# Kernel optimization log

Hardware: AMD Instinct MI355X
Metric: run time of the kernel (lower is better)

The kernel has to match this reference:

```python
import jax, jax.numpy as jnp
import numpy as np
import math

B, N, F, H, T = 2, 1024, 8, 64, 16
E_R, E_C, EA = 8192, 32768, 4
NF = N * F


def _pos_enc(t_steps, h):
    pe = np.zeros((t_steps, h), dtype=np.float32)
    pos = np.arange(t_steps, dtype=np.float32)[:, None]
    div = np.exp(np.arange(0, h, 2, dtype=np.float32) * -(math.log(10000.0) / h))
    pe[:, 0::2] = np.sin(pos * div)
    pe[:, 1::2] = np.cos(pos * div)
    return jnp.asarray(pe)


def _ln(x, g, b, eps=1e-5):
    m = x.mean(-1, keepdims=True)
    v = jnp.var(x, axis=-1, keepdims=True)
    return (x - m) / jnp.sqrt(v + eps) * g + b


def _lrelu(x):
    return jnp.where(x >= 0, x, 0.01 * x)


def setup_inputs() -> dict:
    key = jax.random.key(0)
    ks = jax.random.split(key, 40)
    s = 0.05
    inp = {
        'x_global': jax.random.normal(ks[0], (B, N, H, T), jnp.float32),
        'per_feature_x': jax.random.normal(ks[1], (B, N, F, H, T), jnp.float32),
        'river_edge_attr': jax.random.uniform(ks[2], (E_R, EA), jnp.float32),
        'causal_edge_weight': jax.random.uniform(ks[3], (E_C,), jnp.float32),
        'W_tc': jax.random.normal(ks[4], (H, H, 3), jnp.float32) * s,
        'b_tc': jnp.zeros((H,), jnp.float32),
        'r_lin_W': jax.random.normal(ks[5], (H, H), jnp.float32) * s,
        'r_lin_b': jnp.zeros((H,), jnp.float32),
        'r_upd_W': jax.random.normal(ks[6], (2 * H, H), jnp.float32) * s,
        'r_upd_b': jnp.zeros((H,), jnp.float32),
        'r_edge_W': jax.random.normal(ks[7], (EA, 1), jnp.float32) * s,
        'r_edge_b': jnp.zeros((1,), jnp.float32),
        'r_gate': jnp.ones((1,), jnp.float32) * 0.3,
        'c_lin_W': jax.random.normal(ks[8], (H, H), jnp.float32) * s,
        'c_lin_b': jnp.zeros((H,), jnp.float32),
        'c_upd_W': jax.random.normal(ks[9], (2 * H, H), jnp.float32) * s,
        'c_upd_b': jnp.zeros((H,), jnp.float32),
        'c_gate': jnp.ones((1,), jnp.float32) * 0.3,
        'sf_W': jax.random.normal(ks[10], (2 * H, H), jnp.float32) * s,
        'sf_b': jnp.zeros((H,), jnp.float32),
        'femb': jax.random.normal(ks[11], (F, H), jnp.float32) * 0.02,
        'pfn_g': jnp.ones((H,), jnp.float32),
        'pfn_b': jnp.zeros((H,), jnp.float32),
        'f1_W': jax.random.normal(ks[12], (2 * H, H), jnp.float32) * s,
        'f1_b': jnp.zeros((H,), jnp.float32),
        'fln_g': jnp.ones((H,), jnp.float32),
        'fln_b': jnp.zeros((H,), jnp.float32),
        'f2_W': jax.random.normal(ks[13], (H, H), jnp.float32) * s,
        'f2_b': jnp.zeros((H,), jnp.float32),
        'river_edge_index': jax.random.randint(ks[14], (2, E_R), 0, N, jnp.int64),
        'causal_edge_index': jax.random.randint(ks[15], (2, E_C), 0, NF, jnp.int64),
    }
    return inp


def reference(x_global, per_feature_x, river_edge_attr, causal_edge_weight,
              W_tc, b_tc, r_lin_W, r_lin_b, r_upd_W, r_upd_b, r_edge_W, r_edge_b, r_gate,
              c_lin_W, c_lin_b, c_upd_W, c_upd_b, c_gate, sf_W, sf_b, femb,
              pfn_g, pfn_b, f1_W, f1_b, fln_g, fln_b, f2_W, f2_b,
              river_edge_index, causal_edge_index):
    b_, n_, h_, t_ = x_global.shape
    f_ = per_feature_x.shape[2]
    nf = n_ * f_

    # ---- river graph conv (vectorized over B,T) ----
    x_bt = jnp.transpose(x_global, (0, 3, 1, 2))  # [B,T,N,H]
    ew = (river_edge_attr @ r_edge_W + r_edge_b)[:, 0]  # edge_encoder -> [E_r]
    mw_r = jnp.clip(jax.nn.sigmoid(r_gate) * ew, 0.0, 1.0)
    src_r, tgt_r = river_edge_index[0], river_edge_index[1]
    lx = x_bt @ r_lin_W + r_lin_b
    msg_r = lx[:, :, src_r, :] * mw_r[None, None, :, None]  # [B,T,E_r,H]
    agg_r = jnp.zeros_like(x_bt).at[:, :, tgt_r, :].add(msg_r)
    river_upd = _lrelu(jnp.concatenate([agg_r, x_bt], -1) @ r_upd_W + r_upd_b)

    # ---- causal graph conv on (basin, feature) nodes ----
    pf_bt = jnp.transpose(per_feature_x, (0, 4, 1, 2, 3))  # [B,T,N,F,H]
    nodes = (pf_bt + femb[None, None, None]).reshape(b_, t_, nf, h_)
    mw_c = jnp.clip(jax.nn.sigmoid(c_gate) * causal_edge_weight, 0.0, 1.0)
    src_c, tgt_c = causal_edge_index[0], causal_edge_index[1]
    clx = nodes @ c_lin_W + c_lin_b
    msg_c = clx[:, :, src_c, :] * mw_c[None, None, :, None]  # [B,T,E_c,H]
    agg_c = jnp.zeros_like(nodes).at[:, :, tgt_c, :].add(msg_c)
    cupd = _lrelu(jnp.concatenate([agg_c, nodes], -1) @ c_upd_W + c_upd_b)
    cupd = cupd.reshape(b_, t_, n_, f_, h_)

    # per-feature layernorm over H, then to [B,N,F,H,T]
    pf_out = _ln(cupd, pfn_g, pfn_b)
    pf_out = jnp.transpose(pf_out, (0, 2, 3, 4, 1))

    causal_pooled = cupd.mean(axis=3)  # [B,T,N,H]
    x_spatial = jax.nn.silu(jnp.concatenate([river_upd, causal_pooled], -1) @ sf_W + sf_b)

    # ---- temporal conv with sin/cos positional encoding ----
    pe = _pos_enc(t_, h_)
    xt = jnp.transpose(x_global, (0, 1, 3, 2)) + pe[None, None]  # [B,N,T,H]
    x_nch = jnp.transpose(xt.reshape(b_ * n_, t_, h_), (0, 2, 1))  # [BN,H,T]
    y = jax.lax.conv_general_dilated(x_nch, W_tc, (1,), [(1, 1)],
                                     dimension_numbers=('NCH', 'OIH', 'NCH'))
    y = y + b_tc[None, :, None]
    x_temporal = jnp.transpose(y, (0, 2, 1)).reshape(b_, n_, t_, h_)

    # ---- fusion ----
    x_sp_bnth = jnp.transpose(x_spatial, (0, 2, 1, 3))  # [B,N,T,H]
    fz = jnp.concatenate([x_temporal, x_sp_bnth], -1) @ f1_W + f1_b
    fz = jax.nn.silu(_ln(fz, fln_g, fln_b))
    fz = fz @ f2_W + f2_b
    x_out = jnp.transpose(fz, (0, 1, 3, 2))  # [B,N,H,T]
    return (x_out, pf_out)
```

## Files before the change

### kernel.cpp

```cpp
#include <hip/hip_runtime.h>
#include <cstddef>

#define BB 2
#define NN 1024
#define FF 8
#define HH 64
#define TT 16
#define ER 8192
#define EC 32768
#define EA 4
#define NFD 8192
#define BTT 32
#define LDA 68

__device__ __forceinline__ void tile_gemm(const float* At, const float* Wt,
                                          float4 acc[4], int r0, int c0) {
#pragma unroll 8
  for (int k = 0; k < 64; ++k) {
    float4 a = *(const float4*)(At + k * LDA + r0);
    float4 b = *(const float4*)(Wt + k * LDA + c0);
    acc[0].x = fmaf(a.x, b.x, acc[0].x); acc[0].y = fmaf(a.x, b.y, acc[0].y);
    acc[0].z = fmaf(a.x, b.z, acc[0].z); acc[0].w = fmaf(a.x, b.w, acc[0].w);
    acc[1].x = fmaf(a.y, b.x, acc[1].x); acc[1].y = fmaf(a.y, b.y, acc[1].y);
    acc[1].z = fmaf(a.y, b.z, acc[1].z); acc[1].w = fmaf(a.y, b.w, acc[1].w);
    acc[2].x = fmaf(a.z, b.x, acc[2].x); acc[2].y = fmaf(a.z, b.y, acc[2].y);
    acc[2].z = fmaf(a.z, b.z, acc[2].z); acc[2].w = fmaf(a.z, b.w, acc[2].w);
    acc[3].x = fmaf(a.w, b.x, acc[3].x); acc[3].y = fmaf(a.w, b.y, acc[3].y);
    acc[3].z = fmaf(a.w, b.z, acc[3].z); acc[3].w = fmaf(a.w, b.w, acc[3].w);
  }
}

__device__ __forceinline__ void stage_W(float* Wt, const float* __restrict__ W, int tid) {
#pragma unroll
  for (int q = 0; q < 4; ++q) {
    int i = tid + q * 256;
    int k = i >> 4, c4 = (i & 15) << 2;
    *(float4*)(Wt + k * LDA + c4) = *(const float4*)(W + k * 64 + c4);
  }
}

__device__ __forceinline__ void stage_AT(float* At, const float* __restrict__ src, int tid) {
  int row = tid >> 2, kc = (tid & 3) << 4;
  if (src) {
#pragma unroll
    for (int q = 0; q < 4; ++q) {
      float4 v = *(const float4*)(src + kc + q * 4);
      int k = kc + q * 4;
      At[(k + 0) * LDA + row] = v.x;
      At[(k + 1) * LDA + row] = v.y;
      At[(k + 2) * LDA + row] = v.z;
      At[(k + 3) * LDA + row] = v.w;
    }
  } else {
#pragma unroll
    for (int q = 0; q < 16; ++q) At[(kc + q) * LDA + row] = 0.f;
  }
}

#define FMA4(P, V) \
  P.x = fmaf(w, V.x, P.x); P.y = fmaf(w, V.y, P.y); \
  P.z = fmaf(w, V.z, P.z); P.w = fmaf(w, V.w, P.w);

__device__ __forceinline__ void stage_gather(float* At, float* s_sh,
                                             const float* __restrict__ slice, int rowbase,
                                             const float* __restrict__ mw,
                                             const int* __restrict__ srcarr,
                                             const int* __restrict__ off,
                                             const int* __restrict__ sorted, int tid) {
  int row = tid >> 2, kc = (tid & 3) << 4;
  float4 p0 = make_float4(0.f, 0.f, 0.f, 0.f), p1 = p0, p2 = p0, p3 = p0;
  float s = 0.f;
  int node = rowbase + row;
  int e0 = off[node], e1 = off[node + 1];
  for (int j = e0; j < e1; ++j) {
    int e = sorted[j];
    float w = mw[e];
    const float4* sp = (const float4*)(slice + (size_t)srcarr[e] * 64 + kc);
    float4 v0 = sp[0], v1 = sp[1], v2 = sp[2], v3 = sp[3];
    FMA4(p0, v0); FMA4(p1, v1); FMA4(p2, v2); FMA4(p3, v3);
    s += w;
  }
  At[(kc + 0) * LDA + row] = p0.x;  At[(kc + 1) * LDA + row] = p0.y;
  At[(kc + 2) * LDA + row] = p0.z;  At[(kc + 3) * LDA + row] = p0.w;
  At[(kc + 4) * LDA + row] = p1.x;  At[(kc + 5) * LDA + row] = p1.y;
  At[(kc + 6) * LDA + row] = p1.z;  At[(kc + 7) * LDA + row] = p1.w;
  At[(kc + 8) * LDA + row] = p2.x;  At[(kc + 9) * LDA + row] = p2.y;
  At[(kc + 10) * LDA + row] = p2.z; At[(kc + 11) * LDA + row] = p2.w;
  At[(kc + 12) * LDA + row] = p3.x; At[(kc + 13) * LDA + row] = p3.y;
  At[(kc + 14) * LDA + row] = p3.z; At[(kc + 15) * LDA + row] = p3.w;
  if ((tid & 3) == 0) s_sh[row] = s;
}

__global__ __launch_bounds__(256, 4) void k_gnn(const float* __restrict__ base,
    const int* __restrict__ off, const int* __restrict__ sorted,
    const int* __restrict__ srcarr, const float* __restrict__ mw,
    const float* __restrict__ Wf, const float* __restrict__ Wbot,
    const float* __restrict__ vv, const float* __restrict__ bb,
    float* __restrict__ out, int ngShift, int rowsSlice) {
  __shared__ float At[64 * LDA];
  __shared__ float Wt[64 * LDA];
  __shared__ float s_sh[64];
  int tid = threadIdx.x;
  int bt = blockIdx.x >> ngShift;
  int ng = blockIdx.x & ((1 << ngShift) - 1);
  const float* slice = base + (size_t)bt * rowsSlice * 64;
  int rowbase = ng * 64;
  float4 z4 = make_float4(0.f, 0.f, 0.f, 0.f);
  float4 acc[4] = {z4, z4, z4, z4};
  int r0 = (tid >> 4) << 2, c0 = (tid & 15) << 2;

  stage_W(Wt, Wf, tid);
  stage_gather(At, s_sh, slice, rowbase, mw, srcarr, off, sorted, tid);
  __syncthreads();
  tile_gemm(At, Wt, acc, r0, c0);
  __syncthreads();

  stage_W(Wt, Wbot, tid);
  stage_AT(At, slice + (size_t)(rowbase + (tid >> 2)) * 64, tid);
  __syncthreads();
  tile_gemm(At, Wt, acc, r0, c0);

  float4 v4 = *(const float4*)(vv + c0);
  float4 b4 = *(const float4*)(bb + c0);
#pragma unroll
  for (int i = 0; i < 4; ++i) {
    int row = r0 + i;
    float sv = s_sh[row];
    float4 z;
    z.x = acc[i].x + sv * v4.x + b4.x;
    z.y = acc[i].y + sv * v4.y + b4.y;
    z.z = acc[i].z + sv * v4.z + b4.z;
    z.w = acc[i].w + sv * v4.w + b4.w;
    z.x = z.x >= 0.f ? z.x : 0.01f * z.x;
    z.y = z.y >= 0.f ? z.y : 0.01f * z.y;
    z.z = z.z >= 0.f ? z.z : 0.01f * z.z;
    z.w = z.w >= 0.f ? z.w : 0.01f * z.w;
    *(float4*)(out + ((size_t)bt * rowsSlice + rowbase + row) * 64 + c0) = z;
  }
}

__global__ __launch_bounds__(256, 4) void k_sf2(const float* __restrict__ river_upd,
    const float* __restrict__ pooled, const float* __restrict__ sf_W,
    const float* __restrict__ sf_b, float* __restrict__ x_spatial) {
  __shared__ float At[64 * LDA];
  __shared__ float Wt[64 * LDA];
  int tid = threadIdx.x;
  int rowbase = blockIdx.x * 64;
  float4 z4 = make_float4(0.f, 0.f, 0.f, 0.f);
  float4 acc[4] = {z4, z4, z4, z4};
  int r0 = (tid >> 4) << 2, c0 = (tid & 15) << 2;

  stage_W(Wt, sf_W, tid);
  stage_AT(At, river_upd + (size_t)(rowbase + (tid >> 2)) * 64, tid);
  __syncthreads();
  tile_gemm(At, Wt, acc, r0, c0);
  __syncthreads();

  stage_W(Wt, sf_W + 4096, tid);
  stage_AT(At, pooled + (size_t)(rowbase + (tid >> 2)) * 64, tid);
  __syncthreads();
  tile_gemm(At, Wt, acc, r0, c0);

  float4 b4 = *(const float4*)(sf_b + c0);
#pragma unroll
  for (int i = 0; i < 4; ++i) {
    float4 z;
    z.x = acc[i].x + b4.x; z.y = acc[i].y + b4.y;
    z.z = acc[i].z + b4.z; z.w = acc[i].w + b4.w;
    z.x = z.x / (1.f + expf(-z.x)); z.y = z.y / (1.f + expf(-z.y));
    z.z = z.z / (1.f + expf(-z.z)); z.w = z.w / (1.f + expf(-z.w));
    *(float4*)(x_spatial + (size_t)(rowbase + r0 + i) * 64 + c0) = z;
  }
}

__global__ __launch_bounds__(256, 4) void k_fuse2(const float* __restrict__ xt,
    const float* __restrict__ xsp, const float* __restrict__ Wg,
    const float* __restrict__ cvec, const float* __restrict__ f1W,
    const float* __restrict__ flng, const float* __restrict__ flnb,
    const float* __restrict__ f2W, const float* __restrict__ f2b,
    float* __restrict__ x_out) {
  __shared__ float At[64 * LDA];
  __shared__ float Wt[64 * LDA];
  int tid = threadIdx.x;
  int bn0 = blockIdx.x * 4;
  int srow = tid >> 2;
  int bnl = srow >> 4, t = srow & 15;
  int bn = bn0 + bnl;
  float4 z4 = make_float4(0.f, 0.f, 0.f, 0.f);
  float4 acc[4] = {z4, z4, z4, z4};
  int r0 = (tid >> 4) << 2, c0 = (tid & 15) << 2;

#pragma unroll
  for (int kt = 0; kt < 3; ++kt) {
    int t2 = t + kt - 1;
    const float* src = (t2 >= 0 && t2 < TT) ? xt + ((size_t)bn * TT + t2) * 64 : nullptr;
    stage_W(Wt, Wg + kt * 4096, tid);
    stage_AT(At, src, tid);
    __syncthreads();
    tile_gemm(At, Wt, acc, r0, c0);
    __syncthreads();
  }
  {
    int b = bn >> 10, n = bn & 1023;
    const float* src = xsp + ((size_t)(b * TT + t) * NN + n) * 64;
    stage_W(Wt, f1W + 4096, tid);
    stage_AT(At, src, tid);
    __syncthreads();
    tile_gemm(At, Wt, acc, r0, c0);
    __syncthreads();
  }

  float4 cv = *(const float4*)(cvec + c0);
  float4 g4 = *(const float4*)(flng + c0);
  float4 lb4 = *(const float4*)(flnb + c0);
  float4 zz[4];
#pragma unroll
  for (int i = 0; i < 4; ++i) {
    zz[i].x = acc[i].x + cv.x; zz[i].y = acc[i].y + cv.y;
    zz[i].z = acc[i].z + cv.z; zz[i].w = acc[i].w + cv.w;
    float ps = zz[i].x + zz[i].y + zz[i].z + zz[i].w;
    float pq = zz[i].x * zz[i].x + zz[i].y * zz[i].y + zz[i].z * zz[i].z + zz[i].w * zz[i].w;
    ps += __shfl_xor(ps, 1); pq += __shfl_xor(pq, 1);
    ps += __shfl_xor(ps, 2); pq += __shfl_xor(pq, 2);
    ps += __shfl_xor(ps, 4); pq += __shfl_xor(pq, 4);
    ps += __shfl_xor(ps, 8); pq += __shfl_xor(pq, 8);
    float m = ps * (1.f / 64.f);
    float var = pq * (1.f / 64.f) - m * m;
    float inv = rsqrtf(var + 1e-5f);
    float4 w;
    w.x = (zz[i].x - m) * inv * g4.x + lb4.x;
    w.y = (zz[i].y - m) * inv * g4.y + lb4.y;
    w.z = (zz[i].z - m) * inv * g4.z + lb4.z;
    w.w = (zz[i].w - m) * inv * g4.w + lb4.w;
    zz[i].x = w.x / (1.f + expf(-w.x));
    zz[i].y = w.y / (1.f + expf(-w.y));
    zz[i].z = w.z / (1.f + expf(-w.z));
    zz[i].w = w.w / (1.f + expf(-w.w));
  }
#pragma unroll
  for (int i = 0; i < 4; ++i) {
    At[(c0 + 0) * LDA + r0 + i] = zz[i].x;
    At[(c0 + 1) * LDA + r0 + i] = zz[i].y;
    At[(c0 + 2) * LDA + r0 + i] = zz[i].z;
    At[(c0 + 3) * LDA + r0 + i] = zz[i].w;
  }
  stage_W(Wt, f2W, tid);
  __syncthreads();
  float4 acc2[4] = {z4, z4, z4, z4};
  tile_gemm(At, Wt, acc2, r0, c0);
  __syncthreads();
  float4 f2b4 = *(const float4*)(f2b + c0);
#pragma unroll
  for (int i = 0; i < 4; ++i) {
    float4 o;
    o.x = acc2[i].x + f2b4.x; o.y = acc2[i].y + f2b4.y;
    o.z = acc2[i].z + f2b4.z; o.w = acc2[i].w + f2b4.w;
    *(float4*)(Wt + (r0 + i) * LDA + c0) = o;
  }
  __syncthreads();
#pragma unroll
  for (int q = 0; q < 4; ++q) {
    int idx = tid + q * 256;
    int fo = idx * 4;
    int bnl2 = fo >> 10, rem = fo & 1023;
    int c = rem >> 4, tt = rem & 15;
    float4 o;
    o.x = Wt[(bnl2 * 16 + tt + 0) * LDA + c];
    o.y = Wt[(bnl2 * 16 + tt + 1) * LDA + c];
    o.z = Wt[(bnl2 * 16 + tt + 2) * LDA + c];
    o.w = Wt[(bnl2 * 16 + tt + 3) * LDA + c];
    *(float4*)(x_out + (size_t)(bn0 + bnl2) * 1024 + rem) = o;
  }
}

__global__ void k_prep_edges(const float* __restrict__ attr, const float* __restrict__ cw,
                             const float* __restrict__ reW, const float* __restrict__ reB,
                             const float* __restrict__ rgate, const float* __restrict__ cgate,
                             float* __restrict__ mw_r, float* __restrict__ mw_c,
                             int* __restrict__ rcnt, int* __restrict__ ccnt) {
  int i = blockIdx.x * 256 + threadIdx.x;
  if (i < EC) {
    float g = 1.f / (1.f + expf(-cgate[0]));
    mw_c[i] = fminf(fmaxf(g * cw[i], 0.f), 1.f);
  }
  if (i < ER) {
    float ew = reB[0];
#pragma unroll
    for (int a = 0; a < EA; ++a) ew += attr[i * EA + a] * reW[a];
    float g = 1.f / (1.f + expf(-rgate[0]));
    mw_r[i] = fminf(fmaxf(g * ew, 0.f), 1.f);
  }
  if (i < NN) rcnt[i] = 0;
  if (i < NFD) ccnt[i] = 0;
}

__global__ void k_prep_w(const float* __restrict__ r_lin_W, const float* __restrict__ r_upd_W,
                         const float* __restrict__ r_lin_b,
                         const float* __restrict__ c_lin_W, const float* __restrict__ c_upd_W,
                         const float* __restrict__ c_lin_b,
                         const float* __restrict__ W_tc, const float* __restrict__ b_tc,
                         const float* __restrict__ f1_W, const float* __restrict__ f1_b,
                         float* __restrict__ Wfr, float* __restrict__ v_r,
                         float* __restrict__ Wfc, float* __restrict__ v_c,
                         float* __restrict__ Wg, float* __restrict__ cvec) {
  int tid = threadIdx.x;
  if (blockIdx.x == 0) {
    for (int idx = tid; idx < 4096; idx += 256) {
      int k = idx >> 6, j = idx & 63;
      float s = 0.f;
      for (int m = 0; m < 64; ++m) s += r_lin_W[k * 64 + m] * r_upd_W[m * 64 + j];
      Wfr[idx] = s;
    }
    if (tid < 64) {
      float s = 0.f;
      for (int m = 0; m < 64; ++m) s += r_lin_b[m] * r_upd_W[m * 64 + tid];
      v_r[tid] = s;
    }
  } else if (blockIdx.x == 1) {
    for (int idx = tid; idx < 4096; idx += 256) {
      int k = idx >> 6, j = idx & 63;
      float s = 0.f;
      for (int m = 0; m < 64; ++m) s += c_lin_W[k * 64 + m] * c_upd_W[m * 64 + j];
      Wfc[idx] = s;
    }
    if (tid < 64) {
      float s = 0.f;
      for (int m = 0; m < 64; ++m) s += c_lin_b[m] * c_upd_W[m * 64 + tid];
      v_c[tid] = s;
    }
  } else {
    for (int idx = tid; idx < 12288; idx += 256) {
      int r = idx >> 6, c = idx & 63;
      int kk = r >> 6, i = r & 63;
      float s = 0.f;
      for (int o = 0; o < 64; ++o) s += W_tc[o * 192 + i * 3 + kk] * f1_W[o * 64 + c];
      Wg[idx] = s;
    }
    if (tid < 64) {
      float s = f1_b[tid];
      for (int o = 0; o < 64; ++o) s += b_tc[o] * f1_W[o * 64 + tid];
      cvec[tid] = s;
    }
  }
}

__global__ void k_count(const int* __restrict__ ridx, const int* __restrict__ cidx,
                        int* __restrict__ rcnt, int* __restrict__ ccnt) {
  int e = blockIdx.x * 256 + threadIdx.x;
  if (e < ER) atomicAdd(&rcnt[ridx[ER + e]], 1);
  if (e < EC) atomicAdd(&ccnt[cidx[EC + e]], 1);
}

template <int ITEMS>
__device__ __forceinline__ void scan_impl(const int* __restrict__ cnt, int n,
                                          int* __restrict__ off, int* __restrict__ cur,
                                          int* sh) {
  int tid = threadIdx.x;
  int local[ITEMS];
  int s = 0;
  int base = tid * ITEMS;
#pragma unroll
  for (int j = 0; j < ITEMS; ++j) { local[j] = cnt[base + j]; s += local[j]; }
  sh[tid] = s;
  __syncthreads();
  for (int d = 1; d < 1024; d <<= 1) {
    int v = (tid >= d) ? sh[tid - d] : 0;
    __syncthreads();
    sh[tid] += v;
    __syncthreads();
  }
  int excl = tid ? sh[tid - 1] : 0;
#pragma unroll
  for (int j = 0; j < ITEMS; ++j) { off[base + j] = excl; cur[base + j] = excl; excl += local[j]; }
  if (tid == 1023) off[n] = excl;
}

__global__ __launch_bounds__(1024) void k_scan(const int* __restrict__ rcnt, int* __restrict__ roff,
                                               int* __restrict__ rcur,
                                               const int* __restrict__ ccnt, int* __restrict__ coff,
                                               int* __restrict__ ccur) {
  __shared__ int sh[1024];
  if (blockIdx.x == 0) scan_impl<1>(rcnt, NN, roff, rcur, sh);
  else                 scan_impl<8>(ccnt, NFD, coff, ccur, sh);
}

__global__ void k_fill(const int* __restrict__ ridx, const int* __restrict__ cidx,
                       int* __restrict__ rcur, int* __restrict__ ccur,
                       int* __restrict__ rsorted, int* __restrict__ csorted) {
  int e = blockIdx.x * 256 + threadIdx.x;
  if (e < ER) { int t = ridx[ER + e]; int p = atomicAdd(&rcur[t], 1); rsorted[p] = e; }
  if (e < EC) { int t = cidx[EC + e]; int p = atomicAdd(&ccur[t], 1); csorted[p] = e; }
}

__global__ void k_xpose(const float* __restrict__ xg, float* __restrict__ x_bt,
                        float* __restrict__ xt) {
  __shared__ float lds[64][17];
  int bn = blockIdx.x;
  int b = bn >> 10, n = bn & 1023;
  int tid = threadIdx.x;
  const float* src = xg + (size_t)bn * (HH * TT);
  for (int i = tid; i < 1024; i += 256) lds[i >> 4][i & 15] = src[i];
  __syncthreads();
  for (int i = tid; i < 1024; i += 256) {
    int t = i >> 6, h = i & 63;
    float v = lds[h][t];
    float div = expf(-(float)(h & ~1) * (9.210340371976184f / 64.f));
    float arg = (float)t * div;
    float pe = (h & 1) ? cosf(arg) : sinf(arg);
    xt[(size_t)bn * 1024 + i] = v + pe;
    x_bt[(((size_t)b * TT + t) * NN + n) * HH + h] = v;
  }
}

__global__ void k_nodes(const float* __restrict__ pfx, const float* __restrict__ femb,
                        float* __restrict__ nodes) {
  __shared__ float lds[64][17];
  int bnf = blockIdx.x;
  int f = bnf & 7;
  int n = (bnf >> 3) & 1023;
  int b = bnf >> 13;
  int tid = threadIdx.x;
  const float* src = pfx + (size_t)bnf * (HH * TT);
  for (int i = tid; i < 1024; i += 256) lds[i >> 4][i & 15] = src[i];
  __syncthreads();
  for (int i = tid; i < 1024; i += 256) {
    int t = i >> 6, h = i & 63;
    nodes[(((size_t)b * TT + t) * NFD + n * FF + f) * HH + h] = lds[h][t] + femb[f * HH + h];
  }
}

__global__ void k_pool(const float* __restrict__ cupd, float* __restrict__ pooled) {
  int idx = blockIdx.x * 256 + threadIdx.x;
  int h = idx & 63;
  int n = (idx >> 6) & 1023;
  int bt = idx >> 16;
  const float* base = cupd + ((size_t)bt * NFD + n * FF) * HH + h;
  float s = 0.f;
#pragma unroll
  for (int f = 0; f < FF; ++f) s += base[f * HH];
  pooled[idx] = s * 0.125f;
}

__global__ void k_pfout(const float* __restrict__ cupd, const float* __restrict__ g,
                        const float* __restrict__ be, float* __restrict__ pf_out) {
  __shared__ float lds[16][65];
  __shared__ float mi[16], rs[16];
  int bnf = blockIdx.x;
  int f = bnf & 7;
  int n = (bnf >> 3) & 1023;
  int b = bnf >> 13;
  int tid = threadIdx.x;
  for (int i = tid; i < 1024; i += 256) {
    int t = i >> 6, h = i & 63;
    lds[t][h] = cupd[(((size_t)b * TT + t) * NFD + n * FF + f) * HH + h];
  }
  __syncthreads();
  int t = tid >> 4, l = tid & 15;
  float sm = 0.f;
#pragma unroll
  for (int q = 0; q < 4; ++q) sm += lds[t][l + 16 * q];
  sm += __shfl_xor(sm, 1); sm += __shfl_xor(sm, 2); sm += __shfl_xor(sm, 4); sm += __shfl_xor(sm, 8);
  float m = sm * (1.f / 64.f);
  float sv = 0.f;
#pragma unroll
  for (int q = 0; q < 4; ++q) { float d = lds[t][l + 16 * q] - m; sv += d * d; }
  sv += __shfl_xor(sv, 1); sv += __shfl_xor(sv, 2); sv += __shfl_xor(sv, 4); sv += __shfl_xor(sv, 8);
  float inv = 1.f / sqrtf(sv * (1.f / 64.f) + 1e-5f);
  if (l == 0) { mi[t] = m; rs[t] = inv; }
  __syncthreads();
  float* out = pf_out + (size_t)bnf * (HH * TT);
  for (int i = tid; i < 1024; i += 256) {
    int h = i >> 4, tt = i & 15;
    out[i] = (lds[tt][h] - mi[tt]) * rs[tt] * g[h] + be[h];
  }
}

extern "C" void kernel_launch(void* const* d_in, const int* in_sizes, int n_in,
                              void* d_out, int out_size, void* d_ws, size_t ws_size,
                              hipStream_t stream) {
  (void)in_sizes; (void)n_in; (void)out_size; (void)ws_size;
  const float* x_global     = (const float*)d_in[0];
  const float* per_feature  = (const float*)d_in[1];
  const float* r_edge_attr  = (const float*)d_in[2];
  const float* c_edge_w     = (const float*)d_in[3];
  const float* W_tc         = (const float*)d_in[4];
  const float* b_tc         = (const float*)d_in[5];
  const float* r_lin_W      = (const float*)d_in[6];
  const float* r_lin_b      = (const float*)d_in[7];
  const float* r_upd_W      = (const float*)d_in[8];
  const float* r_upd_b      = (const float*)d_in[9];
  const float* r_edge_W     = (const float*)d_in[10];
  const float* r_edge_b     = (const float*)d_in[11];
  const float* r_gate       = (const float*)d_in[12];
  const float* c_lin_W      = (const float*)d_in[13];
  const float* c_lin_b      = (const float*)d_in[14];
  const float* c_upd_W      = (const float*)d_in[15];
  const float* c_upd_b      = (const float*)d_in[16];
  const float* c_gate       = (const float*)d_in[17];
  const float* sf_W         = (const float*)d_in[18];
  const float* sf_b         = (const float*)d_in[19];
  const float* femb         = (const float*)d_in[20];
  const float* pfn_g        = (const float*)d_in[21];
  const float* pfn_b        = (const float*)d_in[22];
  const float* f1_W         = (const float*)d_in[23];
  const float* f1_b         = (const float*)d_in[24];
  const float* fln_g        = (const float*)d_in[25];
  const float* fln_b        = (const float*)d_in[26];
  const float* f2_W         = (const float*)d_in[27];
  const float* f2_b         = (const float*)d_in[28];
  const int*   ridx         = (const int*)d_in[29];
  const int*   cidx         = (const int*)d_in[30];

  float* out_f = (float*)d_out;
  float* x_out  = out_f;
  float* pf_out = out_f + 2097152;

  const size_t BTNFH = (size_t)BTT * NFD * HH;
  const size_t BTNH  = (size_t)BTT * NN * HH;

  float* ws = (float*)d_ws;
  size_t o = 0;
  float* nodes      = ws + o; o += BTNFH;
  float* cupd       = ws + o; o += BTNFH;
  float* x_bt       = ws + o; o += BTNH;
  float* xt         = ws + o; o += BTNH;
  float* river_upd  = ws + o; o += BTNH;
  float* pooled     = ws + o; o += BTNH;
  float* x_spatial  = ws + o; o += BTNH;
  float* mw_r       = ws + o; o += ER;
  float* mw_c       = ws + o; o += EC;
  float* Wfr        = ws + o; o += 4096;
  float* v_r        = ws + o; o += 64;
  float* Wfc        = ws + o; o += 4096;
  float* v_c        = ws + o; o += 64;
  float* Wg         = ws + o; o += 192 * 64;
  float* cvec       = ws + o; o += 64;
  int* ib = (int*)(ws + o);
  size_t io = 0;
  int* rcnt    = ib + io; io += NN;
  int* roff    = ib + io; io += NN + 1;
  int* rcur    = ib + io; io += NN;
  int* rsorted = ib + io; io += ER;
  int* ccnt    = ib + io; io += NFD;
  int* coff    = ib + io; io += NFD + 1;
  int* ccur    = ib + io; io += NFD;
  int* csorted = ib + io; io += EC;

  k_prep_edges<<<128, 256, 0, stream>>>(r_edge_attr, c_edge_w, r_edge_W, r_edge_b,
                                        r_gate, c_gate, mw_r, mw_c, rcnt, ccnt);
  k_prep_w<<<3, 256, 0, stream>>>(r_lin_W, r_upd_W, r_lin_b, c_lin_W, c_upd_W, c_lin_b,
                                  W_tc, b_tc, f1_W, f1_b, Wfr, v_r, Wfc, v_c, Wg, cvec);
  k_count<<<128, 256, 0, stream>>>(ridx, cidx, rcnt, ccnt);
  k_scan<<<2, 1024, 0, stream>>>(rcnt, roff, rcur, ccnt, coff, ccur);
  k_fill<<<128, 256, 0, stream>>>(ridx, cidx, rcur, ccur, rsorted, csorted);
  k_xpose<<<BB * NN, 256, 0, stream>>>(x_global, x_bt, xt);
  k_nodes<<<BB * NN * FF, 256, 0, stream>>>(per_feature, femb, nodes);
  k_gnn<<<BTT * 16, 256, 0, stream>>>(x_bt, roff, rsorted, ridx, mw_r,
                                      Wfr, r_upd_W + 4096, v_r, r_upd_b,
                                      river_upd, 4, NN);
  k_gnn<<<BTT * 128, 256, 0, stream>>>(nodes, coff, csorted, cidx, mw_c,
                                       Wfc, c_upd_W + 4096, v_c, c_upd_b,
                                       cupd, 7, NFD);
  k_pool<<<8192, 256, 0, stream>>>(cupd, pooled);
  k_pfout<<<BB * NN * FF, 256, 0, stream>>>(cupd, pfn_g, pfn_b, pf_out);
  k_sf2<<<512, 256, 0, stream>>>(river_upd, pooled, sf_W, sf_b, x_spatial);
  k_fuse2<<<512, 256, 0, stream>>>(xt, x_spatial, Wg, cvec, f1_W, fln_g, fln_b,
                                   f2_W, f2_b, x_out);
}
```

Before: 514.1 us.

## Pack edge lists, fuse pooling into GNN, swizzle LDS, remap blocks per XCD

Several changes land at once. Edge source index and weight are packed into one int2 sorted array, which removes the indirect sorted→edge lookups, and the gather loop is unrolled by two. Mean pooling over features is fused into the causal GNN epilogue with shuffles, which drops the separate pool kernel and its reread of cupd. The transposed A tile in LDS gets an XOR swizzle to cut bank conflicts, and block indices are remapped so each XCD handles whole time slices for L2 locality. The packed layout costs slightly more workspace, and the swizzle must match every writer and reader of the A tile.

```diff
diff --git a/kernel.cpp b/kernel.cpp
--- a/kernel.cpp
+++ b/kernel.cpp
@@ -15,9 +15,10 @@
 
 __device__ __forceinline__ void tile_gemm(const float* At, const float* Wt,
                                           float4 acc[4], int r0, int c0) {
-#pragma unroll 8
+#pragma unroll 16
   for (int k = 0; k < 64; ++k) {
-    float4 a = *(const float4*)(At + k * LDA + r0);
+    int rsw = r0 ^ (((k >> 4) & 3) << 2);
+    float4 a = *(const float4*)(At + k * LDA + rsw);
     float4 b = *(const float4*)(Wt + k * LDA + c0);
     acc[0].x = fmaf(a.x, b.x, acc[0].x); acc[0].y = fmaf(a.x, b.y, acc[0].y);
     acc[0].z = fmaf(a.x, b.z, acc[0].z); acc[0].w = fmaf(a.x, b.w, acc[0].w);
@@ -41,19 +42,20 @@
 
 __device__ __forceinline__ void stage_AT(float* At, const float* __restrict__ src, int tid) {
   int row = tid >> 2, kc = (tid & 3) << 4;
+  int rsw = row ^ ((tid & 3) << 2);
   if (src) {
 #pragma unroll
     for (int q = 0; q < 4; ++q) {
       float4 v = *(const float4*)(src + kc + q * 4);
       int k = kc + q * 4;
-      At[(k + 0) * LDA + row] = v.x;
-      At[(k + 1) * LDA + row] = v.y;
-      At[(k + 2) * LDA + row] = v.z;
-      At[(k + 3) * LDA + row] = v.w;
+      At[(k + 0) * LDA + rsw] = v.x;
+      At[(k + 1) * LDA + rsw] = v.y;
+      At[(k + 2) * LDA + rsw] = v.z;
+      At[(k + 3) * LDA + rsw] = v.w;
     }
   } else {
 #pragma unroll
-    for (int q = 0; q < 16; ++q) At[(kc + q) * LDA + row] = 0.f;
+    for (int q = 0; q < 16; ++q) At[(kc + q) * LDA + rsw] = 0.f;
   }
 }
 
@@ -63,46 +65,61 @@
 
 __device__ __forceinline__ void stage_gather(float* At, float* s_sh,
                                              const float* __restrict__ slice, int rowbase,
-                                             const float* __restrict__ mw,
-                                             const int* __restrict__ srcarr,
-                                             const int* __restrict__ off,
-                                             const int* __restrict__ sorted, int tid) {
+                                             const int2* __restrict__ eg,
+                                             const int* __restrict__ off, int tid) {
   int row = tid >> 2, kc = (tid & 3) << 4;
+  int rsw = row ^ ((tid & 3) << 2);
   float4 p0 = make_float4(0.f, 0.f, 0.f, 0.f), p1 = p0, p2 = p0, p3 = p0;
   float s = 0.f;
   int node = rowbase + row;
   int e0 = off[node], e1 = off[node + 1];
-  for (int j = e0; j < e1; ++j) {
-    int e = sorted[j];
-    float w = mw[e];
-    const float4* sp = (const float4*)(slice + (size_t)srcarr[e] * 64 + kc);
-    float4 v0 = sp[0], v1 = sp[1], v2 = sp[2], v3 = sp[3];
-    FMA4(p0, v0); FMA4(p1, v1); FMA4(p2, v2); FMA4(p3, v3);
+  int j = e0;
+  for (; j + 2 <= e1; j += 2) {
+    int2 ea = eg[j], eb = eg[j + 1];
+    float wa = __int_as_float(ea.y), wb = __int_as_float(eb.y);
+    const float4* spa = (const float4*)(slice + (size_t)ea.x * 64 + kc);
+    const float4* spb = (const float4*)(slice + (size_t)eb.x * 64 + kc);
+    float4 a0 = spa[0], a1 = spa[1], a2 = spa[2], a3 = spa[3];
+    float4 b0 = spb[0], b1 = spb[1], b2 = spb[2], b3 = spb[3];
+    { float w = wa; FMA4(p0, a0); FMA4(p1, a1); FMA4(p2, a2); FMA4(p3, a3); }
+    { float w = wb; FMA4(p0, b0); FMA4(p1, b1); FMA4(p2, b2); FMA4(p3, b3); }
+    s += wa + wb;
+  }
+  if (j < e1) {
+    int2 ea = eg[j];
+    float w = __int_as_float(ea.y);
+    const float4* spa = (const float4*)(slice + (size_t)ea.x * 64 + kc);
+    float4 a0 = spa[0], a1 = spa[1], a2 = spa[2], a3 = spa[3];
+    FMA4(p0, a0); FMA4(p1, a1); FMA4(p2, a2); FMA4(p3, a3);
     s += w;
   }
-  At[(kc + 0) * LDA + row] = p0.x;  At[(kc + 1) * LDA + row] = p0.y;
-  At[(kc + 2) * LDA + row] = p0.z;  At[(kc + 3) * LDA + row] = p0.w;
-  At[(kc + 4) * LDA + row] = p1.x;  At[(kc + 5) * LDA + row] = p1.y;
-  At[(kc + 6) * LDA + row] = p1.z;  At[(kc + 7) * LDA + row] = p1.w;
-  At[(kc + 8) * LDA + row] = p2.x;  At[(kc + 9) * LDA + row] = p2.y;
-  At[(kc + 10) * LDA + row] = p2.z; At[(kc + 11) * LDA + row] = p2.w;
-  At[(kc + 12) * LDA + row] = p3.x; At[(kc + 13) * LDA + row] = p3.y;
-  At[(kc + 14) * LDA + row] = p3.z; At[(kc + 15) * LDA + row] = p3.w;
+  At[(kc + 0) * LDA + rsw] = p0.x;  At[(kc + 1) * LDA + rsw] = p0.y;
+  At[(kc + 2) * LDA + rsw] = p0.z;  At[(kc + 3) * LDA + rsw] = p0.w;
+  At[(kc + 4) * LDA + rsw] = p1.x;  At[(kc + 5) * LDA + rsw] = p1.y;
+  At[(kc + 6) * LDA + rsw] = p1.z;  At[(kc + 7) * LDA + rsw] = p1.w;
+  At[(kc + 8) * LDA + rsw] = p2.x;  At[(kc + 9) * LDA + rsw] = p2.y;
+  At[(kc + 10) * LDA + rsw] = p2.z; At[(kc + 11) * LDA + rsw] = p2.w;
+  At[(kc + 12) * LDA + rsw] = p3.x; At[(kc + 13) * LDA + rsw] = p3.y;
+  At[(kc + 14) * LDA + rsw] = p3.z; At[(kc + 15) * LDA + rsw] = p3.w;
   if ((tid & 3) == 0) s_sh[row] = s;
 }
 
+template <bool POOL>
 __global__ __launch_bounds__(256, 4) void k_gnn(const float* __restrict__ base,
-    const int* __restrict__ off, const int* __restrict__ sorted,
-    const int* __restrict__ srcarr, const float* __restrict__ mw,
+    const int* __restrict__ off, const int2* __restrict__ eg,
     const float* __restrict__ Wf, const float* __restrict__ Wbot,
     const float* __restrict__ vv, const float* __restrict__ bb,
-    float* __restrict__ out, int ngShift, int rowsSlice) {
+    float* __restrict__ out, float* __restrict__ pooled,
+    int ngShift, int rowsSlice) {
   __shared__ float At[64 * LDA];
   __shared__ float Wt[64 * LDA];
   __shared__ float s_sh[64];
   int tid = threadIdx.x;
-  int bt = blockIdx.x >> ngShift;
-  int ng = blockIdx.x & ((1 << ngShift) - 1);
+  int bid = blockIdx.x;
+  int xcd = bid & 7;
+  int slot = bid >> 3;
+  int ng = slot & ((1 << ngShift) - 1);
+  int bt = xcd + 8 * (slot >> ngShift);
   const float* slice = base + (size_t)bt * rowsSlice * 64;
   int rowbase = ng * 64;
   float4 z4 = make_float4(0.f, 0.f, 0.f, 0.f);
@@ -110,7 +127,7 @@
   int r0 = (tid >> 4) << 2, c0 = (tid & 15) << 2;
 
   stage_W(Wt, Wf, tid);
-  stage_gather(At, s_sh, slice, rowbase, mw, srcarr, off, sorted, tid);
+  stage_gather(At, s_sh, slice, rowbase, eg, off, tid);
   __syncthreads();
   tile_gemm(At, Wt, acc, r0, c0);
   __syncthreads();
@@ -122,6 +139,7 @@
 
   float4 v4 = *(const float4*)(vv + c0);
   float4 b4 = *(const float4*)(bb + c0);
+  float4 zz[4];
 #pragma unroll
   for (int i = 0; i < 4; ++i) {
     int row = r0 + i;
@@ -135,7 +153,27 @@
     z.y = z.y >= 0.f ? z.y : 0.01f * z.y;
     z.z = z.z >= 0.f ? z.z : 0.01f * z.z;
     z.w = z.w >= 0.f ? z.w : 0.01f * z.w;
+    zz[i] = z;
     *(float4*)(out + ((size_t)bt * rowsSlice + rowbase + row) * 64 + c0) = z;
+  }
+
+  if (POOL) {
+    float4 ps;
+    ps.x = zz[0].x + zz[1].x + zz[2].x + zz[3].x;
+    ps.y = zz[0].y + zz[1].y + zz[2].y + zz[3].y;
+    ps.z = zz[0].z + zz[1].z + zz[2].z + zz[3].z;
+    ps.w = zz[0].w + zz[1].w + zz[2].w + zz[3].w;
+    ps.x += __shfl_xor(ps.x, 16);
+    ps.y += __shfl_xor(ps.y, 16);
+    ps.z += __shfl_xor(ps.z, 16);
+    ps.w += __shfl_xor(ps.w, 16);
+    if (((tid >> 4) & 1) == 0) {
+      int nd = r0 >> 3;
+      float4 o;
+      o.x = ps.x * 0.125f; o.y = ps.y * 0.125f;
+      o.z = ps.z * 0.125f; o.w = ps.w * 0.125f;
+      *(float4*)(pooled + ((size_t)bt * NN + (rowbase >> 3) + nd) * 64 + c0) = o;
+    }
   }
 }
 
@@ -237,12 +275,16 @@
     zz[i].z = w.z / (1.f + expf(-w.z));
     zz[i].w = w.w / (1.f + expf(-w.w));
   }
-#pragma unroll
-  for (int i = 0; i < 4; ++i) {
-    At[(c0 + 0) * LDA + r0 + i] = zz[i].x;
-    At[(c0 + 1) * LDA + r0 + i] = zz[i].y;
-    At[(c0 + 2) * LDA + r0 + i] = zz[i].z;
-    At[(c0 + 3) * LDA + r0 + i] = zz[i].w;
+  {
+    int xsw = ((c0 >> 4) & 3) << 2;
+#pragma unroll
+    for (int i = 0; i < 4; ++i) {
+      int rr = (r0 + i) ^ xsw;
+      At[(c0 + 0) * LDA + rr] = zz[i].x;
+      At[(c0 + 1) * LDA + rr] = zz[i].y;
+      At[(c0 + 2) * LDA + rr] = zz[i].z;
+      At[(c0 + 3) * LDA + rr] = zz[i].w;
+    }
   }
   stage_W(Wt, f2W, tid);
   __syncthreads();
@@ -385,11 +427,18 @@
 }
 
 __global__ void k_fill(const int* __restrict__ ridx, const int* __restrict__ cidx,
+                       const float* __restrict__ mw_r, const float* __restrict__ mw_c,
                        int* __restrict__ rcur, int* __restrict__ ccur,
-                       int* __restrict__ rsorted, int* __restrict__ csorted) {
+                       int2* __restrict__ rpk, int2* __restrict__ cpk) {
   int e = blockIdx.x * 256 + threadIdx.x;
-  if (e < ER) { int t = ridx[ER + e]; int p = atomicAdd(&rcur[t], 1); rsorted[p] = e; }
-  if (e < EC) { int t = cidx[EC + e]; int p = atomicAdd(&ccur[t], 1); csorted[p] = e; }
+  if (e < ER) {
+    int t = ridx[ER + e]; int p = atomicAdd(&rcur[t], 1);
+    rpk[p] = make_int2(ridx[e], __float_as_int(mw_r[e]));
+  }
+  if (e < EC) {
+    int t = cidx[EC + e]; int p = atomicAdd(&ccur[t], 1);
+    cpk[p] = make_int2(cidx[e], __float_as_int(mw_c[e]));
+  }
 }
 
 __global__ void k_xpose(const float* __restrict__ xg, float* __restrict__ x_bt,
@@ -427,18 +476,6 @@
     int t = i >> 6, h = i & 63;
     nodes[(((size_t)b * TT + t) * NFD + n * FF + f) * HH + h] = lds[h][t] + femb[f * HH + h];
   }
-}
-
-__global__ void k_pool(const float* __restrict__ cupd, float* __restrict__ pooled) {
-  int idx = blockIdx.x * 256 + threadIdx.x;
-  int h = idx & 63;
-  int n = (idx >> 6) & 1023;
-  int bt = idx >> 16;
-  const float* base = cupd + ((size_t)bt * NFD + n * FF) * HH + h;
-  float s = 0.f;
-#pragma unroll
-  for (int f = 0; f < FF; ++f) s += base[f * HH];
-  pooled[idx] = s * 0.125f;
 }
 
 __global__ void k_pfout(const float* __restrict__ cupd, const float* __restrict__ g,
@@ -535,16 +572,16 @@
   float* v_c        = ws + o; o += 64;
   float* Wg         = ws + o; o += 192 * 64;
   float* cvec       = ws + o; o += 64;
-  int* ib = (int*)(ws + o);
+  int2* rpk = (int2*)(ws + o);
+  int2* cpk = rpk + ER;
+  int* ib = (int*)(cpk + EC);
   size_t io = 0;
   int* rcnt    = ib + io; io += NN;
   int* roff    = ib + io; io += NN + 1;
-  int* rcur    = ib + io; io += NN;
-  int* rsorted = ib + io; io += ER;
+  int* rcur    = ib + io; io += NN + 1;
   int* ccnt    = ib + io; io += NFD;
   int* coff    = ib + io; io += NFD + 1;
-  int* ccur    = ib + io; io += NFD;
-  int* csorted = ib + io; io += EC;
+  int* ccur    = ib + io; io += NFD + 1;
 
   k_prep_edges<<<128, 256, 0, stream>>>(r_edge_attr, c_edge_w, r_edge_W, r_edge_b,
                                         r_gate, c_gate, mw_r, mw_c, rcnt, ccnt);
@@ -552,16 +589,15 @@
                                   W_tc, b_tc, f1_W, f1_b, Wfr, v_r, Wfc, v_c, Wg, cvec);
   k_count<<<128, 256, 0, stream>>>(ridx, cidx, rcnt, ccnt);
   k_scan<<<2, 1024, 0, stream>>>(rcnt, roff, rcur, ccnt, coff, ccur);
-  k_fill<<<128, 256, 0, stream>>>(ridx, cidx, rcur, ccur, rsorted, csorted);
+  k_fill<<<128, 256, 0, stream>>>(ridx, cidx, mw_r, mw_c, rcur, ccur, rpk, cpk);
   k_xpose<<<BB * NN, 256, 0, stream>>>(x_global, x_bt, xt);
   k_nodes<<<BB * NN * FF, 256, 0, stream>>>(per_feature, femb, nodes);
-  k_gnn<<<BTT * 16, 256, 0, stream>>>(x_bt, roff, rsorted, ridx, mw_r,
-                                      Wfr, r_upd_W + 4096, v_r, r_upd_b,
-                                      river_upd, 4, NN);
-  k_gnn<<<BTT * 128, 256, 0, stream>>>(nodes, coff, csorted, cidx, mw_c,
-                                       Wfc, c_upd_W + 4096, v_c, c_upd_b,
-                                       cupd, 7, NFD);
-  k_pool<<<8192, 256, 0, stream>>>(cupd, pooled);
+  k_gnn<false><<<BTT * 16, 256, 0, stream>>>(x_bt, roff, rpk,
+                                             Wfr, r_upd_W + 4096, v_r, r_upd_b,
+                                             river_upd, nullptr, 4, NN);
+  k_gnn<true><<<BTT * 128, 256, 0, stream>>>(nodes, coff, cpk,
+                                             Wfc, c_upd_W + 4096, v_c, c_upd_b,
+                                             cupd, pooled, 7, NFD);
   k_pfout<<<BB * NN * FF, 256, 0, stream>>>(cupd, pfn_g, pfn_b, pf_out);
   k_sf2<<<512, 256, 0, stream>>>(river_upd, pooled, sf_W, sf_b, x_spatial);
   k_fuse2<<<512, 256, 0, stream>>>(xt, x_spatial, Wg, cvec, f1_W, fln_g, fln_b,
```

Result: faster. 482.1 us (-6.2%).
